# Optimization experiments

Hardware: AMD Instinct MI355X
Metric: run time of the kernel (lower is better)

## Reference

```python
import math
import jax, jax.numpy as jnp
import numpy as np

D = 2048
NH = 16
HD = D // NH
B_IMG = 32
H_ORIG, W_ORIG = 28, 36
POOL = 2
HF, WF = H_ORIG // POOL, W_ORIG // POOL  # 14, 18
T = HF * WF                              # 252 tokens per image
S_TOTAL = B_IMG * T                      # 8064
EPS = 1e-6


def setup_inputs() -> dict:
    key = jax.random.key(0)
    ks = jax.random.split(key, 12)
    w = lambda k, shp: jax.random.normal(k, shp, dtype=jnp.float32) * 0.02
    return {
        'semantic_hidden': jax.random.normal(ks[0], (1, S_TOTAL, D), jnp.float32),
        'vggt_features': jax.random.normal(ks[1], (1, S_TOTAL, D), jnp.float32),
        'grid_thw': jnp.tile(jnp.array([[1, H_ORIG, W_ORIG]], dtype=jnp.int64), (B_IMG, 1)),
        'ln1_w': jnp.ones((D,), jnp.float32), 'ln1_b': jnp.zeros((D,), jnp.float32),
        'ln2_w': jnp.ones((D,), jnp.float32), 'ln2_b': jnp.zeros((D,), jnp.float32),
        'Wq': w(ks[2], (D, D)), 'Wk': w(ks[3], (D, D)),
        'Wv': w(ks[4], (D, D)), 'Wo': w(ks[5], (D, D)),
        'imp_w1': w(ks[6], (D // 4, D)), 'imp_b1': jnp.zeros((D // 4,), jnp.float32),
        'imp_w2': w(ks[7], (1, D // 4)), 'imp_b2': jnp.zeros((1,), jnp.float32),
        'gate_w': w(ks[8], (NH // 2, D)), 'gate_b': jnp.zeros((NH // 2,), jnp.float32),
        'gate': jnp.asarray(0.5, jnp.float32),  # torch init is 0.0 (output would be all-zero); use 0.5 for a meaningful baseline
    }


def _layernorm(x, w, b):
    mu = jnp.mean(x, axis=-1, keepdims=True)
    var = jnp.var(x, axis=-1, keepdims=True)
    return (x - mu) * jax.lax.rsqrt(var + EPS) * w + b


def _spatial_bias(h_feat, w_feat, dtype):
    y = jnp.arange(h_feat, dtype=dtype)
    x = jnp.arange(w_feat, dtype=dtype)
    gy, gx = jnp.meshgrid(y, x, indexing='ij')
    coords = jnp.stack([gy.reshape(-1), gx.reshape(-1)], axis=-1)  # [N, 2]
    diff = coords[:, None, :] - coords[None, :, :]
    dist = jnp.sqrt(jnp.sum(diff * diff, axis=-1))  # [N, N]
    diag_len = math.sqrt(h_feat ** 2 + w_feat ** 2) + 1e-6
    return -dist / diag_len


def reference(semantic_hidden, vggt_features, grid_thw, ln1_w, ln1_b, ln2_w, ln2_b,
              Wq, Wk, Wv, Wo, imp_w1, imp_b1, imp_w2, imp_b2, gate_w, gate_b, gate):
    sem = _layernorm(semantic_hidden, ln1_w, ln1_b)
    vgg = _layernorm(vggt_features, ln2_w, ln2_b)
    B_orig, S_total, Dm = sem.shape

    # grid_thw is a static host constant -> Python ints (shapes must be static)
    h_feat = int(np.asarray(grid_thw)[0, 1]) // POOL
    w_feat = int(np.asarray(grid_thw)[0, 2]) // POOL
    tokens = h_feat * w_feat
    num_images = S_total // tokens

    q_in = sem.reshape(num_images, tokens, Dm)   # [B, S, D]
    kv_in = vgg.reshape(num_images, tokens, Dm)
    B, S = num_images, tokens

    q = (q_in @ Wq.T).reshape(B, S, NH, HD).transpose(0, 2, 1, 3)   # [B, H, S, hd]
    k = (kv_in @ Wk.T).reshape(B, S, NH, HD).transpose(0, 2, 1, 3)
    v = (kv_in @ Wv.T).reshape(B, S, NH, HD).transpose(0, 2, 1, 3)

    attn = jnp.einsum('bhqd,bhkd->bhqk', q, k) / math.sqrt(HD)       # [B, H, S, S]

    # spatial bias on first half of heads, gated per (image, query)
    sp_bias = _spatial_bias(h_feat, w_feat, q.dtype)                 # [S, S]
    gate_score = jax.nn.sigmoid(q_in @ gate_w.T + gate_b)            # [B, S, H/2]
    gate_score = gate_score.transpose(0, 2, 1)[..., None]            # [B, H/2, S, 1]
    split = NH // 2
    attn = attn.at[:, :split].add(sp_bias[None, None] * gate_score)

    # importance gate: log-importance bias over keys, shared across heads
    hidden = jax.nn.relu(q_in @ imp_w1.T + imp_b1)
    importance = jax.nn.sigmoid(hidden @ imp_w2.T + imp_b2)          # [B, S, 1]
    attn = attn + jnp.log(importance + 0.1).reshape(B, 1, 1, S)

    probs = jax.nn.softmax(attn, axis=-1)
    out = jnp.einsum('bhqk,bhkd->bhqd', probs, v)                    # [B, H, S, hd]
    out = out.transpose(0, 2, 1, 3).reshape(B, S, Dm)
    out = out.reshape(B_orig, S_total, Dm) @ Wo.T
    return jnp.tanh(gate) * out
```

## Files before the change

kernel.cpp:

```cpp
#include <hip/hip_runtime.h>
#include <hip/hip_bf16.h>
#include <math.h>

typedef __bf16 bf16_t;
typedef __bf16 bf16x8 __attribute__((ext_vector_type(8)));
typedef float f32x4v __attribute__((ext_vector_type(4)));
typedef unsigned short ushort_t;

#define SL_TOTAL 8064
#define DMODEL 2048
#define NHEAD 16
#define HDIM 128
#define SEQ 252

__device__ __forceinline__ bf16_t f2bf(float f) {
  unsigned u = __builtin_bit_cast(unsigned, f);
  u += 0x7fffu + ((u >> 16) & 1u);
  ushort_t h = (ushort_t)(u >> 16);
  return __builtin_bit_cast(bf16_t, h);
}
__device__ __forceinline__ float bf2f(bf16_t b) {
  unsigned u = ((unsigned)__builtin_bit_cast(ushort_t, b)) << 16;
  return __builtin_bit_cast(float, u);
}

__global__ __launch_bounds__(256) void cvt_kernel(const float* __restrict__ src,
                                                  bf16_t* __restrict__ dst, int n) {
  int i = (blockIdx.x * 256 + threadIdx.x) * 8;
  if (i >= n) return;
  float4 a = *(const float4*)(src + i);
  float4 b = *(const float4*)(src + i + 4);
  bf16x8 o;
  o[0] = f2bf(a.x); o[1] = f2bf(a.y); o[2] = f2bf(a.z); o[3] = f2bf(a.w);
  o[4] = f2bf(b.x); o[5] = f2bf(b.y); o[6] = f2bf(b.z); o[7] = f2bf(b.w);
  *(bf16x8*)(dst + i) = o;
}

__global__ __launch_bounds__(256) void ln_kernel(
    const float* __restrict__ sem, const float* __restrict__ vgg,
    const float* __restrict__ w1, const float* __restrict__ b1,
    const float* __restrict__ w2, const float* __restrict__ b2,
    bf16_t* __restrict__ o1, bf16_t* __restrict__ o2) {
  const float* x; const float* w; const float* bb; bf16_t* o;
  int row = blockIdx.x;
  if (blockIdx.y == 0) { x = sem; w = w1; bb = b1; o = o1; }
  else                 { x = vgg; w = w2; bb = b2; o = o2; }
  x += (size_t)row * DMODEL; o += (size_t)row * DMODEL;
  int t = threadIdx.x, wid = t >> 6, lane = t & 63;
  float4 va = *(const float4*)(x + t * 8);
  float4 vb = *(const float4*)(x + t * 8 + 4);
  float s  = va.x + va.y + va.z + va.w + vb.x + vb.y + vb.z + vb.w;
  float ss = va.x*va.x + va.y*va.y + va.z*va.z + va.w*va.w
           + vb.x*vb.x + vb.y*vb.y + vb.z*vb.z + vb.w*vb.w;
  #pragma unroll
  for (int m = 1; m < 64; m <<= 1) { s += __shfl_xor(s, m); ss += __shfl_xor(ss, m); }
  __shared__ float rs[4], rss[4];
  if (lane == 0) { rs[wid] = s; rss[wid] = ss; }
  __syncthreads();
  float st = rs[0] + rs[1] + rs[2] + rs[3];
  float sst = rss[0] + rss[1] + rss[2] + rss[3];
  float mu = st * (1.0f / 2048.0f);
  float var = sst * (1.0f / 2048.0f) - mu * mu;
  float rstd = rsqrtf(var + 1e-6f);
  float4 wa = *(const float4*)(w + t * 8);
  float4 wb = *(const float4*)(w + t * 8 + 4);
  float4 ba = *(const float4*)(bb + t * 8);
  float4 bb4 = *(const float4*)(bb + t * 8 + 4);
  bf16x8 ov;
  ov[0] = f2bf((va.x - mu) * rstd * wa.x + ba.x);
  ov[1] = f2bf((va.y - mu) * rstd * wa.y + ba.y);
  ov[2] = f2bf((va.z - mu) * rstd * wa.z + ba.z);
  ov[3] = f2bf((va.w - mu) * rstd * wa.w + ba.w);
  ov[4] = f2bf((vb.x - mu) * rstd * wb.x + bb4.x);
  ov[5] = f2bf((vb.y - mu) * rstd * wb.y + bb4.y);
  ov[6] = f2bf((vb.z - mu) * rstd * wb.z + bb4.z);
  ov[7] = f2bf((vb.w - mu) * rstd * wb.w + bb4.w);
  *(bf16x8*)(o + t * 8) = ov;
}

template <int EPI>
__global__ __launch_bounds__(256, 2) void gemm_bt(
    const bf16_t* __restrict__ A, const bf16_t* __restrict__ B,
    void* __restrict__ C, void* __restrict__ C2,
    const float* __restrict__ bias, const float* __restrict__ gatep,
    int M, int N, int K, int nnt) {
  __shared__ bf16_t As[2][128 * 64];
  __shared__ bf16_t Bs[2][128 * 64];
  const int nblk = gridDim.x;
  const int orig = blockIdx.x;
  const int qd = nblk >> 3, rr = nblk & 7, xc = orig & 7, lin = orig >> 3;
  const int wg = (xc < rr ? xc * (qd + 1) : rr * (qd + 1) + (xc - rr) * qd) + lin;
  const int mtile = wg / nnt;
  const int ntile = wg - mtile * nnt;
  const int m0 = mtile * 128, n0 = ntile * 128;

  const int tid = threadIdx.x;
  const int wid = tid >> 6, lane = tid & 63;
  const int l15 = lane & 15, l4 = lane >> 4;
  const int wm = (wid >> 1) * 64, wn = (wid & 1) * 64;
  const int srow = lane >> 3;
  const int scol = 8 * ((lane & 7) ^ (lane >> 3));

  f32x4v acc[4][4] = {};
  const int nkt = K >> 6;

  auto stage = [&](int kt, int buf) {
    const int k0 = kt << 6;
    #pragma unroll
    for (int it = 0; it < 4; ++it) {
      int chunk = wid + 4 * it;
      int row = chunk * 8 + srow;
      const bf16_t* ga = A + (size_t)(m0 + row) * K + k0 + scol;
      const bf16_t* gb = B + (size_t)(n0 + row) * K + k0 + scol;
      bf16_t* la = &As[buf][chunk * 512];
      bf16_t* lb = &Bs[buf][chunk * 512];
      __builtin_amdgcn_global_load_lds((const __attribute__((address_space(1))) unsigned int*)ga,
                                       (__attribute__((address_space(3))) unsigned int*)la, 16, 0, 0);
      __builtin_amdgcn_global_load_lds((const __attribute__((address_space(1))) unsigned int*)gb,
                                       (__attribute__((address_space(3))) unsigned int*)lb, 16, 0, 0);
    }
  };

  stage(0, 0);
  for (int kt = 0; kt < nkt; ++kt) {
    int buf = kt & 1;
    __syncthreads();
    if (kt + 1 < nkt) stage(kt + 1, buf ^ 1);
    const char* as = (const char*)As[buf];
    const char* bs = (const char*)Bs[buf];
    #pragma unroll
    for (int ki = 0; ki < 2; ++ki) {
      int cb = ki * 64 + l4 * 16;
      bf16x8 af[4], bfv[4];
      #pragma unroll
      for (int mi = 0; mi < 4; ++mi) {
        int row = wm + mi * 16 + l15;
        af[mi] = *(const bf16x8*)(as + row * 128 + (cb ^ ((row & 7) << 4)));
      }
      #pragma unroll
      for (int ni = 0; ni < 4; ++ni) {
        int row = wn + ni * 16 + l15;
        bfv[ni] = *(const bf16x8*)(bs + row * 128 + (cb ^ ((row & 7) << 4)));
      }
      #pragma unroll
      for (int mi = 0; mi < 4; ++mi)
        #pragma unroll
        for (int ni = 0; ni < 4; ++ni)
          acc[mi][ni] = __builtin_amdgcn_mfma_f32_16x16x32_bf16(af[mi], bfv[ni], acc[mi][ni], 0, 0, 0);
    }
    __syncthreads();
  }

  float scale = 1.0f;
  if (EPI == 2) scale = tanhf(gatep[0]);
  bf16_t* Cb = (bf16_t*)C;
  int colbase = n0;
  int ldc = N;
  if (EPI == 3) {
    ldc = 2048;
    if (n0 >= 2048) { Cb = (bf16_t*)C2; colbase = n0 - 2048; }
  }
  #pragma unroll
  for (int mi = 0; mi < 4; ++mi) {
    #pragma unroll
    for (int ni = 0; ni < 4; ++ni) {
      int c = colbase + wn + ni * 16 + l15;
      #pragma unroll
      for (int j = 0; j < 4; ++j) {
        int r = m0 + wm + mi * 16 + 4 * l4 + j;
        float v = acc[mi][ni][j];
        if (EPI == 1) { v += bias[c]; v = v > 0.0f ? v : 0.0f; }
        if (EPI == 2) ((float*)C)[(size_t)r * N + c] = v * scale;
        else Cb[(size_t)r * ldc + c] = f2bf(v);
      }
    }
  }
}

__global__ __launch_bounds__(256) void gate_kernel(const bf16_t* __restrict__ a,
                                                   const float* __restrict__ gw,
                                                   const float* __restrict__ gb,
                                                   float* __restrict__ gs) {
  int row = blockIdx.x;
  int t = threadIdx.x;
  int j = t >> 5, lt = t & 31;
  const bf16_t* ar = a + (size_t)row * DMODEL;
  const float* wr = gw + (size_t)j * DMODEL;
  float sum = 0.0f;
  #pragma unroll
  for (int u = 0; u < 8; ++u) {
    int i = lt * 8 + u * 256;
    bf16x8 av = *(const bf16x8*)(ar + i);
    float4 w0 = *(const float4*)(wr + i);
    float4 w1 = *(const float4*)(wr + i + 4);
    sum += bf2f(av[0]) * w0.x + bf2f(av[1]) * w0.y + bf2f(av[2]) * w0.z + bf2f(av[3]) * w0.w
         + bf2f(av[4]) * w1.x + bf2f(av[5]) * w1.y + bf2f(av[6]) * w1.z + bf2f(av[7]) * w1.w;
  }
  #pragma unroll
  for (int m = 1; m < 32; m <<= 1) sum += __shfl_xor(sum, m);
  if (lt == 0) gs[(size_t)row * 8 + j] = 1.0f / (1.0f + __expf(-(sum + gb[j])));
}

__global__ __launch_bounds__(256) void imp_kernel(const bf16_t* __restrict__ hid,
                                                  const float* __restrict__ w2,
                                                  const float* __restrict__ b2,
                                                  float* __restrict__ kb) {
  int row = blockIdx.x * 4 + (threadIdx.x >> 6);
  int lane = threadIdx.x & 63;
  const bf16_t* hr = hid + (size_t)row * 512;
  bf16x8 hv = *(const bf16x8*)(hr + lane * 8);
  float sum = 0.0f;
  #pragma unroll
  for (int i = 0; i < 8; ++i) sum += bf2f(hv[i]) * w2[lane * 8 + i];
  #pragma unroll
  for (int m = 1; m < 64; m <<= 1) sum += __shfl_xor(sum, m);
  if (lane == 0) {
    float imp = 1.0f / (1.0f + __expf(-(sum + b2[0])));
    kb[row] = logf(imp + 0.1f);
  }
}

__global__ __launch_bounds__(512, 1) void attn_kernel(
    const bf16_t* __restrict__ Q, const bf16_t* __restrict__ K,
    const bf16_t* __restrict__ V, const float* __restrict__ gs,
    const float* __restrict__ kb, bf16_t* __restrict__ O) {
  __shared__ bf16_t Kt[64 * 128];
  __shared__ bf16_t Vt[128 * 64];
  __shared__ bf16_t Pl[8][32 * 72];
  __shared__ float kyf[256], kxf[256], kbl[256];

  const int bi = blockIdx.x >> 4;
  const int h = blockIdx.x & 15;
  const int tid = threadIdx.x;
  const int wid = tid >> 6;
  const int lane = tid & 63;
  const int l15 = lane & 15, l4 = lane >> 4;
  const bool hs = (h < 8);

  for (int i = tid; i < 256; i += 512) {
    kyf[i] = (float)(i / 18);
    kxf[i] = (float)(i % 18);
    int kk = i < SEQ ? i : SEQ - 1;
    kbl[i] = kb[bi * SEQ + kk];
  }

  const int q0 = wid * 32;
  bf16x8 qf[2][4];
  #pragma unroll
  for (int mi = 0; mi < 2; ++mi) {
    int q = q0 + mi * 16 + l15; if (q >= SEQ) q = SEQ - 1;
    const bf16_t* qp = Q + (size_t)(bi * SEQ + q) * DMODEL + h * HDIM;
    #pragma unroll
    for (int ki = 0; ki < 4; ++ki) qf[mi][ki] = *(const bf16x8*)(qp + ki * 32 + l4 * 8);
  }

  float gsv[2][4], qyv[2][4], qxv[2][4];
  #pragma unroll
  for (int mi = 0; mi < 2; ++mi)
    #pragma unroll
    for (int j = 0; j < 4; ++j) {
      int q = q0 + mi * 16 + 4 * l4 + j;
      int qc = q < SEQ ? q : SEQ - 1;
      gsv[mi][j] = hs ? gs[(size_t)(bi * SEQ + qc) * 8 + h] : 0.0f;
      qyv[mi][j] = (float)(q / 18);
      qxv[mi][j] = (float)(q % 18);
    }

  float mrow[2][4], lrow[2][4];
  #pragma unroll
  for (int mi = 0; mi < 2; ++mi)
    #pragma unroll
    for (int j = 0; j < 4; ++j) { mrow[mi][j] = -3.0e38f; lrow[mi][j] = 0.0f; }

  f32x4v oacc[2][8] = {};
  const float scl = 0.08838834764831845f;
  const float invdiag = 1.0f / (sqrtf(520.0f) + 1e-6f);
  bf16_t* Plw = &Pl[wid][0];

  for (int t = 0; t < 4; ++t) {
    __syncthreads();
    #pragma unroll
    for (int rep = 0; rep < 2; ++rep) {
      int s = tid + rep * 512;
      int row = s >> 4, cb = s & 15;
      int kk = t * 64 + row;
      uint4 val = make_uint4(0, 0, 0, 0);
      if (kk < SEQ) val = *(const uint4*)(K + (size_t)(bi * SEQ + kk) * DMODEL + h * HDIM + cb * 8);
      *(uint4*)((char*)Kt + row * 256 + ((cb * 16) ^ ((row & 7) << 4))) = val;
    }
    {
      int kp = tid >> 4, db = tid & 15;
      int k0i = t * 64 + kp * 2, k1i = k0i + 1;
      uint4 a = make_uint4(0, 0, 0, 0), c4 = make_uint4(0, 0, 0, 0);
      if (k0i < SEQ) a = *(const uint4*)(V + (size_t)(bi * SEQ + k0i) * DMODEL + h * HDIM + db * 8);
      if (k1i < SEQ) c4 = *(const uint4*)(V + (size_t)(bi * SEQ + k1i) * DMODEL + h * HDIM + db * 8);
      const ushort_t* au = (const ushort_t*)&a;
      const ushort_t* cu = (const ushort_t*)&c4;
      #pragma unroll
      for (int i = 0; i < 8; ++i) {
        int d = db * 8 + i;
        unsigned pv = (unsigned)au[i] | ((unsigned)cu[i] << 16);
        *(unsigned*)((char*)Vt + d * 128 + ((kp * 4) ^ ((d & 7) << 4))) = pv;
      }
    }
    __syncthreads();

    f32x4v sc[2][4] = {};
    #pragma unroll
    for (int ki = 0; ki < 4; ++ki) {
      bf16x8 kf[4];
      #pragma unroll
      for (int ni = 0; ni < 4; ++ni) {
        int row = ni * 16 + l15;
        kf[ni] = *(const bf16x8*)((char*)Kt + row * 256 + ((ki * 64 + l4 * 16) ^ ((row & 7) << 4)));
      }
      #pragma unroll
      for (int mi = 0; mi < 2; ++mi)
        #pragma unroll
        for (int ni = 0; ni < 4; ++ni)
          sc[mi][ni] = __builtin_amdgcn_mfma_f32_16x16x32_bf16(qf[mi][ki], kf[ni], sc[mi][ni], 0, 0, 0);
    }

    #pragma unroll
    for (int mi = 0; mi < 2; ++mi) {
      #pragma unroll
      for (int j = 0; j < 4; ++j) {
        float s4[4];
        float rm = -3.0e38f;
        #pragma unroll
        for (int ni = 0; ni < 4; ++ni) {
          int kk = t * 64 + ni * 16 + l15;
          float s = sc[mi][ni][j] * scl + kbl[kk];
          if (hs) {
            float dy = qyv[mi][j] - kyf[kk];
            float dx = qxv[mi][j] - kxf[kk];
            s -= sqrtf(dy * dy + dx * dx) * invdiag * gsv[mi][j];
          }
          if (kk >= SEQ) s = -3.0e38f;
          s4[ni] = s;
          rm = fmaxf(rm, s);
        }
        #pragma unroll
        for (int msk = 1; msk < 16; msk <<= 1) rm = fmaxf(rm, __shfl_xor(rm, msk));
        float mold = mrow[mi][j];
        float mnew = fmaxf(mold, rm);
        float corr = __expf(mold - mnew);
        float rsum = 0.0f;
        #pragma unroll
        for (int ni = 0; ni < 4; ++ni) {
          float p = __expf(s4[ni] - mnew);
          s4[ni] = p;
          rsum += p;
        }
        #pragma unroll
        for (int msk = 1; msk < 16; msk <<= 1) rsum += __shfl_xor(rsum, msk);
        mrow[mi][j] = mnew;
        lrow[mi][j] = lrow[mi][j] * corr + rsum;
        #pragma unroll
        for (int di = 0; di < 8; ++di) oacc[mi][di][j] *= corr;
        int prow = mi * 16 + 4 * l4 + j;
        #pragma unroll
        for (int ni = 0; ni < 4; ++ni)
          Plw[prow * 72 + ni * 16 + l15] = f2bf(s4[ni]);
      }
    }

    #pragma unroll
    for (int ks = 0; ks < 2; ++ks) {
      bf16x8 pf[2];
      #pragma unroll
      for (int mi = 0; mi < 2; ++mi)
        pf[mi] = *(const bf16x8*)(Plw + (mi * 16 + l15) * 72 + ks * 32 + l4 * 8);
      #pragma unroll
      for (int di = 0; di < 8; ++di) {
        int d = di * 16 + l15;
        bf16x8 vf = *(const bf16x8*)((char*)Vt + d * 128 + ((ks * 64 + l4 * 16) ^ ((d & 7) << 4)));
        #pragma unroll
        for (int mi = 0; mi < 2; ++mi)
          oacc[mi][di] = __builtin_amdgcn_mfma_f32_16x16x32_bf16(pf[mi], vf, oacc[mi][di], 0, 0, 0);
      }
    }
  }

  #pragma unroll
  for (int mi = 0; mi < 2; ++mi) {
    #pragma unroll
    for (int j = 0; j < 4; ++j) {
      int q = q0 + mi * 16 + 4 * l4 + j;
      if (q >= SEQ) continue;
      float inv = 1.0f / lrow[mi][j];
      bf16_t* op = O + (size_t)(bi * SEQ + q) * DMODEL + h * HDIM;
      #pragma unroll
      for (int di = 0; di < 8; ++di)
        op[di * 16 + l15] = f2bf(oacc[mi][di][j] * inv);
    }
  }
}

extern "C" void kernel_launch(void* const* d_in, const int* in_sizes, int n_in,
                              void* d_out, int out_size, void* d_ws, size_t ws_size,
                              hipStream_t stream) {
  const float* sem  = (const float*)d_in[0];
  const float* vgg  = (const float*)d_in[1];
  const float* ln1w = (const float*)d_in[3];
  const float* ln1b = (const float*)d_in[4];
  const float* ln2w = (const float*)d_in[5];
  const float* ln2b = (const float*)d_in[6];
  const float* Wq   = (const float*)d_in[7];
  const float* Wk   = (const float*)d_in[8];
  const float* Wv   = (const float*)d_in[9];
  const float* Wo   = (const float*)d_in[10];
  const float* w1   = (const float*)d_in[11];
  const float* b1   = (const float*)d_in[12];
  const float* w2   = (const float*)d_in[13];
  const float* b2   = (const float*)d_in[14];
  const float* gw   = (const float*)d_in[15];
  const float* gb   = (const float*)d_in[16];
  const float* gate = (const float*)d_in[17];

  char* ws = (char*)d_ws;
  const size_t SZ_W = 8388608;
  const size_t SZ_ACT = 33030144;
  bf16_t* Wqb  = (bf16_t*)(ws + 0);
  bf16_t* Wkb  = (bf16_t*)(ws + SZ_W);
  bf16_t* Wvb  = (bf16_t*)(ws + 2 * SZ_W);
  bf16_t* Wob  = (bf16_t*)(ws + 3 * SZ_W);
  bf16_t* w1b  = (bf16_t*)(ws + 4 * SZ_W);
  bf16_t* semb = (bf16_t*)(ws + 4 * SZ_W + 2097152);
  bf16_t* vggb = (bf16_t*)(ws + 4 * SZ_W + 2097152 + SZ_ACT);
  bf16_t* Vb   = (bf16_t*)(ws + 4 * SZ_W + 2097152 + 2 * SZ_ACT);
  bf16_t* hidb = (bf16_t*)(ws + 4 * SZ_W + 2097152 + 3 * SZ_ACT);
  float*  gsb  = (float*)(ws + 4 * SZ_W + 2097152 + 3 * SZ_ACT + 8257536);
  float*  kbb  = (float*)(ws + 4 * SZ_W + 2097152 + 3 * SZ_ACT + 8257536 + 258048);
  bf16_t* Qb = (bf16_t*)d_out;
  bf16_t* Kb = (bf16_t*)((char*)d_out + SZ_ACT);
  bf16_t* attnb = semb;

  cvt_kernel<<<2048, 256, 0, stream>>>(Wq, Wqb, 4194304);
  cvt_kernel<<<2048, 256, 0, stream>>>(Wk, Wkb, 4194304);
  cvt_kernel<<<2048, 256, 0, stream>>>(Wv, Wvb, 4194304);
  cvt_kernel<<<2048, 256, 0, stream>>>(Wo, Wob, 4194304);
  cvt_kernel<<<512, 256, 0, stream>>>(w1, w1b, 1048576);
  ln_kernel<<<dim3(8064, 2), 256, 0, stream>>>(sem, vgg, ln1w, ln1b, ln2w, ln2b, semb, vggb);

  gemm_bt<0><<<1008, 256, 0, stream>>>(semb, Wqb, Qb, nullptr, nullptr, nullptr,
                                       8064, 2048, 2048, 16);
  gemm_bt<3><<<2016, 256, 0, stream>>>(vggb, Wkb, Kb, Vb, nullptr, nullptr,
                                       8064, 4096, 2048, 32);
  gemm_bt<1><<<252, 256, 0, stream>>>(semb, w1b, hidb, nullptr, b1, nullptr,
                                      8064, 512, 2048, 4);

  gate_kernel<<<8064, 256, 0, stream>>>(semb, gw, gb, gsb);
  imp_kernel<<<2016, 256, 0, stream>>>(hidb, w2, b2, kbb);

  attn_kernel<<<512, 512, 0, stream>>>(Qb, Kb, Vb, gsb, kbb, attnb);

  gemm_bt<2><<<1008, 256, 0, stream>>>(attnb, Wob, d_out, nullptr, nullptr, gate,
                                       8064, 2048, 2048, 16);
}
```

Baseline: 532.9 us.

## Shrink GEMM K-tile, batch gate rows, drop online-softmax max, merge weight converts

```diff
diff --git a/kernel.cpp b/kernel.cpp
--- a/kernel.cpp
+++ b/kernel.cpp
@@ -8,6 +8,7 @@
 typedef unsigned short ushort_t;
 
 #define SL_TOTAL 8064
+#define SL_PAD 8192
 #define DMODEL 2048
 #define NHEAD 16
 #define HDIM 128
@@ -22,6 +23,30 @@
 __device__ __forceinline__ float bf2f(bf16_t b) {
   unsigned u = ((unsigned)__builtin_bit_cast(ushort_t, b)) << 16;
   return __builtin_bit_cast(float, u);
+}
+
+__global__ __launch_bounds__(256) void cvt4_kernel(const float* __restrict__ s0,
+                                                   const float* __restrict__ s1,
+                                                   const float* __restrict__ s2,
+                                                   const float* __restrict__ s3,
+                                                   bf16_t* __restrict__ d0,
+                                                   bf16_t* __restrict__ d1,
+                                                   bf16_t* __restrict__ d2,
+                                                   bf16_t* __restrict__ d3) {
+  const float* src; bf16_t* dst;
+  switch (blockIdx.y) {
+    case 0: src = s0; dst = d0; break;
+    case 1: src = s1; dst = d1; break;
+    case 2: src = s2; dst = d2; break;
+    default: src = s3; dst = d3; break;
+  }
+  int i = (blockIdx.x * 256 + threadIdx.x) * 8;
+  float4 a = *(const float4*)(src + i);
+  float4 b = *(const float4*)(src + i + 4);
+  bf16x8 o;
+  o[0] = f2bf(a.x); o[1] = f2bf(a.y); o[2] = f2bf(a.z); o[3] = f2bf(a.w);
+  o[4] = f2bf(b.x); o[5] = f2bf(b.y); o[6] = f2bf(b.z); o[7] = f2bf(b.w);
+  *(bf16x8*)(dst + i) = o;
 }
 
 __global__ __launch_bounds__(256) void cvt_kernel(const float* __restrict__ src,
@@ -79,45 +104,42 @@
 }
 
 template <int EPI>
-__global__ __launch_bounds__(256, 2) void gemm_bt(
+__global__ __launch_bounds__(256, 4) void gemm128(
     const bf16_t* __restrict__ A, const bf16_t* __restrict__ B,
     void* __restrict__ C, void* __restrict__ C2,
     const float* __restrict__ bias, const float* __restrict__ gatep,
-    int M, int N, int K, int nnt) {
-  __shared__ bf16_t As[2][128 * 64];
-  __shared__ bf16_t Bs[2][128 * 64];
+    int Mreal, int N, int K, int nnt) {
+  __shared__ bf16_t As[2][128 * 32];
+  __shared__ bf16_t Bs[2][128 * 32];
   const int nblk = gridDim.x;
   const int orig = blockIdx.x;
   const int qd = nblk >> 3, rr = nblk & 7, xc = orig & 7, lin = orig >> 3;
   const int wg = (xc < rr ? xc * (qd + 1) : rr * (qd + 1) + (xc - rr) * qd) + lin;
-  const int mtile = wg / nnt;
-  const int ntile = wg - mtile * nnt;
+  const int mtile = wg / nnt, ntile = wg - mtile * nnt;
   const int m0 = mtile * 128, n0 = ntile * 128;
 
   const int tid = threadIdx.x;
   const int wid = tid >> 6, lane = tid & 63;
   const int l15 = lane & 15, l4 = lane >> 4;
   const int wm = (wid >> 1) * 64, wn = (wid & 1) * 64;
-  const int srow = lane >> 3;
-  const int scol = 8 * ((lane & 7) ^ (lane >> 3));
+  const int srow = lane >> 2;
+  const int scol = 8 * ((lane & 3) ^ (srow & 3));
 
   f32x4v acc[4][4] = {};
-  const int nkt = K >> 6;
+  const int nkt = K >> 5;
 
   auto stage = [&](int kt, int buf) {
-    const int k0 = kt << 6;
-    #pragma unroll
-    for (int it = 0; it < 4; ++it) {
-      int chunk = wid + 4 * it;
-      int row = chunk * 8 + srow;
+    const int k0 = kt << 5;
+    #pragma unroll
+    for (int q = 0; q < 2; ++q) {
+      int chunk = wid * 2 + q;
+      int row = chunk * 16 + srow;
       const bf16_t* ga = A + (size_t)(m0 + row) * K + k0 + scol;
       const bf16_t* gb = B + (size_t)(n0 + row) * K + k0 + scol;
-      bf16_t* la = &As[buf][chunk * 512];
-      bf16_t* lb = &Bs[buf][chunk * 512];
       __builtin_amdgcn_global_load_lds((const __attribute__((address_space(1))) unsigned int*)ga,
-                                       (__attribute__((address_space(3))) unsigned int*)la, 16, 0, 0);
+          (__attribute__((address_space(3))) unsigned int*)(&As[buf][chunk * 512]), 16, 0, 0);
       __builtin_amdgcn_global_load_lds((const __attribute__((address_space(1))) unsigned int*)gb,
-                                       (__attribute__((address_space(3))) unsigned int*)lb, 16, 0, 0);
+          (__attribute__((address_space(3))) unsigned int*)(&Bs[buf][chunk * 512]), 16, 0, 0);
     }
   };
 
@@ -128,26 +150,22 @@
     if (kt + 1 < nkt) stage(kt + 1, buf ^ 1);
     const char* as = (const char*)As[buf];
     const char* bs = (const char*)Bs[buf];
-    #pragma unroll
-    for (int ki = 0; ki < 2; ++ki) {
-      int cb = ki * 64 + l4 * 16;
-      bf16x8 af[4], bfv[4];
-      #pragma unroll
-      for (int mi = 0; mi < 4; ++mi) {
-        int row = wm + mi * 16 + l15;
-        af[mi] = *(const bf16x8*)(as + row * 128 + (cb ^ ((row & 7) << 4)));
-      }
-      #pragma unroll
-      for (int ni = 0; ni < 4; ++ni) {
-        int row = wn + ni * 16 + l15;
-        bfv[ni] = *(const bf16x8*)(bs + row * 128 + (cb ^ ((row & 7) << 4)));
-      }
-      #pragma unroll
-      for (int mi = 0; mi < 4; ++mi)
-        #pragma unroll
-        for (int ni = 0; ni < 4; ++ni)
-          acc[mi][ni] = __builtin_amdgcn_mfma_f32_16x16x32_bf16(af[mi], bfv[ni], acc[mi][ni], 0, 0, 0);
-    }
+    bf16x8 af[4], bfv[4];
+    #pragma unroll
+    for (int mi = 0; mi < 4; ++mi) {
+      int row = wm + mi * 16 + l15;
+      af[mi] = *(const bf16x8*)(as + row * 64 + ((l4 ^ (row & 3)) << 4));
+    }
+    #pragma unroll
+    for (int ni = 0; ni < 4; ++ni) {
+      int row = wn + ni * 16 + l15;
+      bfv[ni] = *(const bf16x8*)(bs + row * 64 + ((l4 ^ (row & 3)) << 4));
+    }
+    #pragma unroll
+    for (int mi = 0; mi < 4; ++mi)
+      #pragma unroll
+      for (int ni = 0; ni < 4; ++ni)
+        acc[mi][ni] = __builtin_amdgcn_mfma_f32_16x16x32_bf16(af[mi], bfv[ni], acc[mi][ni], 0, 0, 0);
     __syncthreads();
   }
 
@@ -168,6 +186,7 @@
       #pragma unroll
       for (int j = 0; j < 4; ++j) {
         int r = m0 + wm + mi * 16 + 4 * l4 + j;
+        if (r >= Mreal) continue;
         float v = acc[mi][ni][j];
         if (EPI == 1) { v += bias[c]; v = v > 0.0f ? v : 0.0f; }
         if (EPI == 2) ((float*)C)[(size_t)r * N + c] = v * scale;
@@ -181,24 +200,33 @@
                                                    const float* __restrict__ gw,
                                                    const float* __restrict__ gb,
                                                    float* __restrict__ gs) {
-  int row = blockIdx.x;
+  int r0 = blockIdx.x * 4;
   int t = threadIdx.x;
   int j = t >> 5, lt = t & 31;
-  const bf16_t* ar = a + (size_t)row * DMODEL;
   const float* wr = gw + (size_t)j * DMODEL;
-  float sum = 0.0f;
+  float sum[4] = {0.0f, 0.0f, 0.0f, 0.0f};
   #pragma unroll
   for (int u = 0; u < 8; ++u) {
     int i = lt * 8 + u * 256;
-    bf16x8 av = *(const bf16x8*)(ar + i);
     float4 w0 = *(const float4*)(wr + i);
     float4 w1 = *(const float4*)(wr + i + 4);
-    sum += bf2f(av[0]) * w0.x + bf2f(av[1]) * w0.y + bf2f(av[2]) * w0.z + bf2f(av[3]) * w0.w
-         + bf2f(av[4]) * w1.x + bf2f(av[5]) * w1.y + bf2f(av[6]) * w1.z + bf2f(av[7]) * w1.w;
-  }
-  #pragma unroll
-  for (int m = 1; m < 32; m <<= 1) sum += __shfl_xor(sum, m);
-  if (lt == 0) gs[(size_t)row * 8 + j] = 1.0f / (1.0f + __expf(-(sum + gb[j])));
+    #pragma unroll
+    for (int r = 0; r < 4; ++r) {
+      bf16x8 av = *(const bf16x8*)(a + (size_t)(r0 + r) * DMODEL + i);
+      sum[r] += bf2f(av[0]) * w0.x + bf2f(av[1]) * w0.y + bf2f(av[2]) * w0.z + bf2f(av[3]) * w0.w
+              + bf2f(av[4]) * w1.x + bf2f(av[5]) * w1.y + bf2f(av[6]) * w1.z + bf2f(av[7]) * w1.w;
+    }
+  }
+  #pragma unroll
+  for (int m = 1; m < 32; m <<= 1) {
+    #pragma unroll
+    for (int r = 0; r < 4; ++r) sum[r] += __shfl_xor(sum[r], m);
+  }
+  if (lt == 0) {
+    #pragma unroll
+    for (int r = 0; r < 4; ++r)
+      gs[(size_t)(r0 + r) * 8 + j] = 1.0f / (1.0f + __expf(-(sum[r] + gb[j])));
+  }
 }
 
 __global__ __launch_bounds__(256) void imp_kernel(const bf16_t* __restrict__ hid,
@@ -254,28 +282,26 @@
     for (int ki = 0; ki < 4; ++ki) qf[mi][ki] = *(const bf16x8*)(qp + ki * 32 + l4 * 8);
   }
 
-  float gsv[2][4], qyv[2][4], qxv[2][4];
+  const float invdiag = 1.0f / (sqrtf(520.0f) + 1e-6f);
+  float gsd[2][4], qyv[2][4], qxv[2][4];
   #pragma unroll
   for (int mi = 0; mi < 2; ++mi)
     #pragma unroll
     for (int j = 0; j < 4; ++j) {
       int q = q0 + mi * 16 + 4 * l4 + j;
       int qc = q < SEQ ? q : SEQ - 1;
-      gsv[mi][j] = hs ? gs[(size_t)(bi * SEQ + qc) * 8 + h] : 0.0f;
+      gsd[mi][j] = hs ? gs[(size_t)(bi * SEQ + qc) * 8 + h] * invdiag : 0.0f;
       qyv[mi][j] = (float)(q / 18);
       qxv[mi][j] = (float)(q % 18);
     }
 
-  float mrow[2][4], lrow[2][4];
-  #pragma unroll
-  for (int mi = 0; mi < 2; ++mi)
-    #pragma unroll
-    for (int j = 0; j < 4; ++j) { mrow[mi][j] = -3.0e38f; lrow[mi][j] = 0.0f; }
-
   f32x4v oacc[2][8] = {};
+  f32x4v osum[2] = {};
   const float scl = 0.08838834764831845f;
-  const float invdiag = 1.0f / (sqrtf(520.0f) + 1e-6f);
   bf16_t* Plw = &Pl[wid][0];
+  bf16x8 vones;
+  #pragma unroll
+  for (int i = 0; i < 8; ++i) vones[i] = f2bf(1.0f);
 
   for (int t = 0; t < 4; ++t) {
     __syncthreads();
@@ -325,8 +351,7 @@
     for (int mi = 0; mi < 2; ++mi) {
       #pragma unroll
       for (int j = 0; j < 4; ++j) {
-        float s4[4];
-        float rm = -3.0e38f;
+        int prow = mi * 16 + 4 * l4 + j;
         #pragma unroll
         for (int ni = 0; ni < 4; ++ni) {
           int kk = t * 64 + ni * 16 + l15;
@@ -334,34 +359,11 @@
           if (hs) {
             float dy = qyv[mi][j] - kyf[kk];
             float dx = qxv[mi][j] - kxf[kk];
-            s -= sqrtf(dy * dy + dx * dx) * invdiag * gsv[mi][j];
+            s -= sqrtf(dy * dy + dx * dx) * gsd[mi][j];
           }
-          if (kk >= SEQ) s = -3.0e38f;
-          s4[ni] = s;
-          rm = fmaxf(rm, s);
+          float p = (kk < SEQ) ? __expf(s) : 0.0f;
+          Plw[prow * 72 + ni * 16 + l15] = f2bf(p);
         }
-        #pragma unroll
-        for (int msk = 1; msk < 16; msk <<= 1) rm = fmaxf(rm, __shfl_xor(rm, msk));
-        float mold = mrow[mi][j];
-        float mnew = fmaxf(mold, rm);
-        float corr = __expf(mold - mnew);
-        float rsum = 0.0f;
-        #pragma unroll
-        for (int ni = 0; ni < 4; ++ni) {
-          float p = __expf(s4[ni] - mnew);
-          s4[ni] = p;
-          rsum += p;
-        }
-        #pragma unroll
-        for (int msk = 1; msk < 16; msk <<= 1) rsum += __shfl_xor(rsum, msk);
-        mrow[mi][j] = mnew;
-        lrow[mi][j] = lrow[mi][j] * corr + rsum;
-        #pragma unroll
-        for (int di = 0; di < 8; ++di) oacc[mi][di][j] *= corr;
-        int prow = mi * 16 + 4 * l4 + j;
-        #pragma unroll
-        for (int ni = 0; ni < 4; ++ni)
-          Plw[prow * 72 + ni * 16 + l15] = f2bf(s4[ni]);
       }
     }
 
@@ -371,6 +373,9 @@
       #pragma unroll
       for (int mi = 0; mi < 2; ++mi)
         pf[mi] = *(const bf16x8*)(Plw + (mi * 16 + l15) * 72 + ks * 32 + l4 * 8);
+      #pragma unroll
+      for (int mi = 0; mi < 2; ++mi)
+        osum[mi] = __builtin_amdgcn_mfma_f32_16x16x32_bf16(pf[mi], vones, osum[mi], 0, 0, 0);
       #pragma unroll
       for (int di = 0; di < 8; ++di) {
         int d = di * 16 + l15;
@@ -388,7 +393,7 @@
     for (int j = 0; j < 4; ++j) {
       int q = q0 + mi * 16 + 4 * l4 + j;
       if (q >= SEQ) continue;
-      float inv = 1.0f / lrow[mi][j];
+      float inv = 1.0f / osum[mi][j];
       bf16_t* op = O + (size_t)(bi * SEQ + q) * DMODEL + h * HDIM;
       #pragma unroll
       for (int di = 0; di < 8; ++di)
@@ -419,42 +424,40 @@
   const float* gate = (const float*)d_in[17];
 
   char* ws = (char*)d_ws;
-  const size_t SZ_W = 8388608;
-  const size_t SZ_ACT = 33030144;
+  const size_t SZ_W    = 8388608;
+  const size_t SZ_PAD  = 33554432;
+  const size_t SZ_ACT  = 33030144;
   bf16_t* Wqb  = (bf16_t*)(ws + 0);
   bf16_t* Wkb  = (bf16_t*)(ws + SZ_W);
   bf16_t* Wvb  = (bf16_t*)(ws + 2 * SZ_W);
   bf16_t* Wob  = (bf16_t*)(ws + 3 * SZ_W);
   bf16_t* w1b  = (bf16_t*)(ws + 4 * SZ_W);
   bf16_t* semb = (bf16_t*)(ws + 4 * SZ_W + 2097152);
-  bf16_t* vggb = (bf16_t*)(ws + 4 * SZ_W + 2097152 + SZ_ACT);
-  bf16_t* Vb   = (bf16_t*)(ws + 4 * SZ_W + 2097152 + 2 * SZ_ACT);
-  bf16_t* hidb = (bf16_t*)(ws + 4 * SZ_W + 2097152 + 3 * SZ_ACT);
-  float*  gsb  = (float*)(ws + 4 * SZ_W + 2097152 + 3 * SZ_ACT + 8257536);
-  float*  kbb  = (float*)(ws + 4 * SZ_W + 2097152 + 3 * SZ_ACT + 8257536 + 258048);
+  bf16_t* vggb = (bf16_t*)(ws + 4 * SZ_W + 2097152 + SZ_PAD);
+  bf16_t* Vb   = (bf16_t*)(ws + 4 * SZ_W + 2097152 + 2 * SZ_PAD);
+  bf16_t* hidb = (bf16_t*)(ws + 4 * SZ_W + 2097152 + 2 * SZ_PAD + SZ_ACT);
+  float*  gsb  = (float*)(ws + 4 * SZ_W + 2097152 + 2 * SZ_PAD + SZ_ACT + 8257536);
+  float*  kbb  = (float*)(ws + 4 * SZ_W + 2097152 + 2 * SZ_PAD + SZ_ACT + 8257536 + 258048);
   bf16_t* Qb = (bf16_t*)d_out;
   bf16_t* Kb = (bf16_t*)((char*)d_out + SZ_ACT);
   bf16_t* attnb = semb;
 
-  cvt_kernel<<<2048, 256, 0, stream>>>(Wq, Wqb, 4194304);
-  cvt_kernel<<<2048, 256, 0, stream>>>(Wk, Wkb, 4194304);
-  cvt_kernel<<<2048, 256, 0, stream>>>(Wv, Wvb, 4194304);
-  cvt_kernel<<<2048, 256, 0, stream>>>(Wo, Wob, 4194304);
+  cvt4_kernel<<<dim3(2048, 4), 256, 0, stream>>>(Wq, Wk, Wv, Wo, Wqb, Wkb, Wvb, Wob);
   cvt_kernel<<<512, 256, 0, stream>>>(w1, w1b, 1048576);
   ln_kernel<<<dim3(8064, 2), 256, 0, stream>>>(sem, vgg, ln1w, ln1b, ln2w, ln2b, semb, vggb);
 
-  gemm_bt<0><<<1008, 256, 0, stream>>>(semb, Wqb, Qb, nullptr, nullptr, nullptr,
+  gemm128<0><<<1024, 256, 0, stream>>>(semb, Wqb, Qb, nullptr, nullptr, nullptr,
                                        8064, 2048, 2048, 16);
-  gemm_bt<3><<<2016, 256, 0, stream>>>(vggb, Wkb, Kb, Vb, nullptr, nullptr,
+  gemm128<3><<<2048, 256, 0, stream>>>(vggb, Wkb, Kb, Vb, nullptr, nullptr,
                                        8064, 4096, 2048, 32);
-  gemm_bt<1><<<252, 256, 0, stream>>>(semb, w1b, hidb, nullptr, b1, nullptr,
+  gemm128<1><<<256, 256, 0, stream>>>(semb, w1b, hidb, nullptr, b1, nullptr,
                                       8064, 512, 2048, 4);
 
-  gate_kernel<<<8064, 256, 0, stream>>>(semb, gw, gb, gsb);
+  gate_kernel<<<2016, 256, 0, stream>>>(semb, gw, gb, gsb);
   imp_kernel<<<2016, 256, 0, stream>>>(hidb, w2, b2, kbb);
 
   attn_kernel<<<512, 512, 0, stream>>>(Qb, Kb, Vb, gsb, kbb, attnb);
 
-  gemm_bt<2><<<1008, 256, 0, stream>>>(attnb, Wob, d_out, nullptr, nullptr, gate,
+  gemm128<2><<<1024, 256, 0, stream>>>(attnb, Wob, d_out, nullptr, nullptr, gate,
                                        8064, 2048, 2048, 16);
 }
```

After: 515.5 us. 3.3% less time.
